# Kernel tuning notes

Hardware: AMD Instinct MI355X
Metric: run time of the kernel (lower is better)

Reference implementation:

```python
import jax, jax.numpy as jnp
import numpy as np

N = 100000   # num_nodes
E = 1250000  # num_edges
D = 64       # embedding_dim
L = 3        # num_layers


def setup_inputs() -> dict:
    key = jax.random.key(0)
    k1, k2, k3, k4 = jax.random.split(key, 4)
    edge_index = jax.random.randint(k1, (2, E), 0, N, dtype=jnp.int64)
    edge_label_index = jax.random.randint(k2, (2, E), 0, N, dtype=jnp.int64)
    # xavier_uniform init of Embedding(N, D)
    bound = float(np.sqrt(6.0 / (N + D)))
    emb_weight = jax.random.uniform(k3, (N, D), jnp.float32, -bound, bound)
    alpha = jnp.full((L + 1,), 1.0 / (L + 1), dtype=jnp.float32)
    return {"edge_index": edge_index, "edge_label_index": edge_label_index,
            "emb_weight": emb_weight, "alpha": alpha}


def reference(edge_index, edge_label_index, emb_weight, alpha):
    src, dst = edge_index[0], edge_index[1]
    n = emb_weight.shape[0]
    # gcn_norm (LGConv, no self-loops): deg over destination, sym normalization
    deg = jax.ops.segment_sum(jnp.ones(src.shape[0], emb_weight.dtype), dst, num_segments=n)
    dis = jnp.where(deg > 0, jax.lax.rsqrt(jnp.where(deg > 0, deg, 1.0)), 0.0)
    w = dis[src] * dis[dst]  # [E]

    weights = jax.nn.softmax(alpha)  # [L+1]
    x = emb_weight
    out = x * weights[0]
    for i in range(L):
        # LGConv: out[dst] += norm * x[src]
        x = jax.ops.segment_sum(w[:, None] * x[src], dst, num_segments=n)
        out = out + x * weights[i + 1]

    # predict_link_embedding: per-edge dot product
    return (out[edge_label_index[0]] * out[edge_label_index[1]]).sum(axis=-1)
```

## Files before the change

kernel.cpp:

```cpp
#include <hip/hip_runtime.h>
#include <math.h>

#define DIM 64
#define PART_T 4096
#define BK_SHIFT 9
#define BK_SPAN 512
#define BK_CAP 8192
#define BK_PAD 2048
#define BK_REG (BK_CAP + BK_PAD)

typedef _Float16 half8 __attribute__((ext_vector_type(8)));


__device__ __forceinline__ half8 shfl_xor_h8(half8 v, int mask) {
    int4 iv;
    __builtin_memcpy(&iv, &v, 16);
    iv.x = __shfl_xor(iv.x, mask, 64);
    iv.y = __shfl_xor(iv.y, mask, 64);
    iv.z = __shfl_xor(iv.z, mask, 64);
    iv.w = __shfl_xor(iv.w, mask, 64);
    half8 r;
    __builtin_memcpy(&r, &iv, 16);
    return r;
}

__device__ __forceinline__ half8 dpp_ror8_h8(half8 v) {
    int4 iv;
    __builtin_memcpy(&iv, &v, 16);
    int4 r;
    r.x = __builtin_amdgcn_update_dpp(0, iv.x, 0x128, 0xF, 0xF, true);
    r.y = __builtin_amdgcn_update_dpp(0, iv.y, 0x128, 0xF, 0xF, true);
    r.z = __builtin_amdgcn_update_dpp(0, iv.z, 0x128, 0xF, 0xF, true);
    r.w = __builtin_amdgcn_update_dpp(0, iv.w, 0x128, 0xF, 0xF, true);
    half8 out;
    __builtin_memcpy(&out, &r, 16);
    return out;
}

__device__ __forceinline__ float dpp_sum8_f32(float v) {
    int x = __float_as_int(v);
    v += __int_as_float(__builtin_amdgcn_update_dpp(0, x, 0xB1, 0xF, 0xF, true));
    x = __float_as_int(v);
    v += __int_as_float(__builtin_amdgcn_update_dpp(0, x, 0x4E, 0xF, 0xF, true));
    x = __float_as_int(v);
    v += __int_as_float(__builtin_amdgcn_update_dpp(0, x, 0x141, 0xF, 0xF, true));
    return v;
}

__device__ __forceinline__ int wave_incl_scan(int v) {
    int lane = threadIdx.x & 63;
    #pragma unroll
    for (int d = 1; d < 64; d <<= 1) {
        int n = __shfl_up(v, d, 64);
        if (lane >= d) v += n;
    }
    return v;
}

__device__ __forceinline__ int block_scan_excl(int v, int* wsum) {
    int incl = wave_incl_scan(v);
    int w = threadIdx.x >> 6;
    if ((threadIdx.x & 63) == 63) wsum[w] = incl;
    __syncthreads();
    int offset = 0;
    #pragma unroll
    for (int i = 0; i < 3; ++i) offset += (i < w) ? wsum[i] : 0;
    return offset + incl - v;
}


__global__ void init_kernel(int* __restrict__ gcursor, int K,
                            half8* __restrict__ g0, half8* __restrict__ g1,
                            half8* __restrict__ g2, int N) {
    int t = threadIdx.x;
    if (t < K) gcursor[t] = t * BK_CAP;
    if (t < 8) {
        half8 z = (half8)(_Float16)0;
        g0[(size_t)N * 8 + t] = z;
        g1[(size_t)N * 8 + t] = z;
        g2[(size_t)N * 8 + t] = z;
    }
}


__global__ void part_kernel(const int* __restrict__ src, const int* __restrict__ dst,
                            int* __restrict__ gcursor, unsigned int* __restrict__ part,
                            int E, int K) {
    __shared__ unsigned int tmp_rec[PART_T];
    __shared__ unsigned int reord[PART_T];
    __shared__ unsigned char tmp_bkt[PART_T];
    __shared__ unsigned char tmp_bkt2[PART_T];
    __shared__ int hist[256];
    __shared__ int lstart[256];
    __shared__ int cursor[256];
    __shared__ int gbase[256];
    __shared__ int wsum[4];
    int t = threadIdx.x;
    int tile = blockIdx.x * PART_T;
    int n = E - tile; if (n > PART_T) n = PART_T;

    hist[t] = 0;
    __syncthreads();

    for (int i = t; i < n; i += 256) {
        int s = src[tile + i];
        int d = dst[tile + i];
        int b = d >> BK_SHIFT;
        tmp_rec[i] = (unsigned int)s | ((unsigned int)(d & (BK_SPAN - 1)) << 17);
        tmp_bkt[i] = (unsigned char)b;
        atomicAdd(&hist[b], 1);
    }
    __syncthreads();

    int hv = hist[t];
    int excl = block_scan_excl(hv, wsum);
    lstart[t] = excl;
    cursor[t] = excl;
    if (t < K && hv > 0) gbase[t] = atomicAdd(&gcursor[t], hv);
    __syncthreads();

    for (int i = t; i < n; i += 256) {
        int b = tmp_bkt[i];
        int r = atomicAdd(&cursor[b], 1);
        reord[r] = tmp_rec[i];
        tmp_bkt2[r] = (unsigned char)b;
    }
    __syncthreads();

    for (int i = t; i < n; i += 256) {
        int b = tmp_bkt2[i];
        part[gbase[b] + (i - lstart[b])] = reord[i];
    }
}


__global__ void csr_kernel(const unsigned int* __restrict__ part, const int* __restrict__ gcursor,
                           int2* __restrict__ prange, int* __restrict__ csr_src,
                           float* __restrict__ dis,
                           const float* __restrict__ emb, half8* __restrict__ g0, int N) {
    __shared__ int h[BK_SPAN];
    __shared__ int pfx[BK_SPAN + 1];
    __shared__ float sdis[BK_SPAN];
    __shared__ int wsum[4];
    int b = blockIdx.x;
    int t = threadIdx.x;
    int pbase = b * BK_CAP;
    int cnt   = gcursor[b] - pbase;
    int qbase = b * BK_REG;
    int nodeBase = b << BK_SHIFT;

    h[t] = 0; h[t + 256] = 0;
    __syncthreads();

    for (int j = t; j < cnt; j += 256) {
        unsigned int rec = part[pbase + j];
        atomicAdd(&h[rec >> 17], 1);
    }
    __syncthreads();

    int d0 = h[2 * t], d1 = h[2 * t + 1];
    {
        float f0 = d0 > 0 ? rsqrtf((float)d0) : 0.0f;
        float f1 = d1 > 0 ? rsqrtf((float)d1) : 0.0f;
        int i0 = nodeBase + 2 * t, i1 = i0 + 1;
        if (i0 < N) dis[i0] = f0;
        if (i1 < N) dis[i1] = f1;
        sdis[2 * t] = f0;
        sdis[2 * t + 1] = f1;
    }
    int p0 = (d0 + 3) & ~3;
    int p1 = (d1 + 3) & ~3;
    int excl = block_scan_excl(p0 + p1, wsum);
    pfx[2 * t]     = excl;
    pfx[2 * t + 1] = excl + p0;
    h[2 * t]       = excl;
    h[2 * t + 1]   = excl + p0;
    if (t == 255) pfx[BK_SPAN] = excl + p0 + p1;
    __syncthreads();

    #pragma unroll
    for (int k = 0; k < 2; ++k) {
        int i = t + k * 256;
        int idx = nodeBase + i;
        if (idx < N) prange[idx] = make_int2(qbase + pfx[i], qbase + pfx[i + 1]);
    }
    __syncthreads();

    for (int j = t; j < cnt; j += 256) {
        unsigned int rec = part[pbase + j];
        int dl = (int)(rec >> 17);
        int s  = (int)(rec & 0x1FFFFu);
        int p = atomicAdd(&h[dl], 1);
        csr_src[qbase + p] = s;
    }
    __syncthreads();

    #pragma unroll
    for (int k = 0; k < 2; ++k) {
        int i = t + k * 256;
        int endp = pfx[i + 1];
        for (int p = h[i]; p < endp; ++p) csr_src[qbase + p] = N;
    }

    const float4* e4 = (const float4*)emb;
    int nloc = N - nodeBase;
    if (nloc > BK_SPAN) nloc = BK_SPAN;
    int lim = nloc * 8;
    for (int j = t; j < lim; j += 256) {
        int r = j >> 3;
        int v = nodeBase + r;
        float dv = sdis[r];
        float4 a = e4[(size_t)v * 16 + (size_t)(j & 7) * 2];
        float4 c = e4[(size_t)v * 16 + (size_t)(j & 7) * 2 + 1];
        half8 hh;
        hh[0] = (_Float16)(dv * a.x); hh[1] = (_Float16)(dv * a.y);
        hh[2] = (_Float16)(dv * a.z); hh[3] = (_Float16)(dv * a.w);
        hh[4] = (_Float16)(dv * c.x); hh[5] = (_Float16)(dv * c.y);
        hh[6] = (_Float16)(dv * c.z); hh[7] = (_Float16)(dv * c.w);
        g0[(size_t)v * 8 + (j & 7)] = hh;
    }
}


__device__ __forceinline__ void softmax4(const float* __restrict__ alpha, float* w) {
    float a0 = alpha[0], a1 = alpha[1], a2 = alpha[2], a3 = alpha[3];
    float m = fmaxf(fmaxf(a0, a1), fmaxf(a2, a3));
    float e0 = expf(a0 - m), e1 = expf(a1 - m), e2 = expf(a2 - m), e3 = expf(a3 - m);
    float s = 1.0f / (e0 + e1 + e2 + e3);
    w[0] = e0 * s; w[1] = e1 * s; w[2] = e2 * s; w[3] = e3 * s;
}

__global__ void spmm_kernel(const int2* __restrict__ prange, const int* __restrict__ csr_src,
                            const float* __restrict__ dis,
                            const half8* __restrict__ gin, half8* __restrict__ gout, int N) {
    int lane = threadIdx.x & 63;
    int wave = blockIdx.x * (blockDim.x >> 6) + (threadIdx.x >> 6);
    int v = wave * 2 + (lane >> 5);
    int slot = (lane >> 3) & 3;
    int sub  = lane & 7;
    bool valid = v < N;
    int beg = 0, end = 0;
    if (valid) { int2 pr = prange[v]; beg = pr.x; end = pr.y; }
    const int4* csr4 = (const int4*)csr_src;
    half8 acc0 = (half8)(_Float16)0;
    half8 acc1 = (half8)(_Float16)0;
    for (int j = beg + slot * 4; j < end; j += 16) {
        int4 c = csr4[j >> 2];
        acc0 = acc0 + gin[c.x * 8 + sub];
        acc1 = acc1 + gin[c.y * 8 + sub];
        acc0 = acc0 + gin[c.z * 8 + sub];
        acc1 = acc1 + gin[c.w * 8 + sub];
    }
    half8 acc = acc0 + acc1;
    acc = acc + dpp_ror8_h8(acc);
    acc = acc + shfl_xor_h8(acc, 16);
    if (valid && (lane & 31) < 8) {
        float d = dis[v];
        float d2 = d * d;
        half8 o;
        #pragma unroll
        for (int k = 0; k < 8; ++k) o[k] = (_Float16)(d2 * (float)acc[k]);
        gout[v * 8 + sub] = o;
    }
}

__global__ void spmm_final_kernel(const int2* __restrict__ prange, const int* __restrict__ csr_src,
                                  const float* __restrict__ dis,
                                  const float* __restrict__ emb, const half8* __restrict__ g1,
                                  const half8* __restrict__ g2, half8* __restrict__ out,
                                  const float* __restrict__ alpha, int N) {
    int lane = threadIdx.x & 63;
    int wave = blockIdx.x * (blockDim.x >> 6) + (threadIdx.x >> 6);
    int v = wave * 2 + (lane >> 5);
    int slot = (lane >> 3) & 3;
    int sub  = lane & 7;
    bool valid = v < N;
    int beg = 0, end = 0;
    if (valid) { int2 pr = prange[v]; beg = pr.x; end = pr.y; }
    const int4* csr4 = (const int4*)csr_src;
    half8 acc0 = (half8)(_Float16)0;
    half8 acc1 = (half8)(_Float16)0;
    for (int j = beg + slot * 4; j < end; j += 16) {
        int4 c = csr4[j >> 2];
        acc0 = acc0 + g2[c.x * 8 + sub];
        acc1 = acc1 + g2[c.y * 8 + sub];
        acc0 = acc0 + g2[c.z * 8 + sub];
        acc1 = acc1 + g2[c.w * 8 + sub];
    }
    half8 acc = acc0 + acc1;
    acc = acc + dpp_ror8_h8(acc);
    acc = acc + shfl_xor_h8(acc, 16);
    if (valid && (lane & 31) < 8) {
        float w[4];
        softmax4(alpha, w);
        float d  = dis[v];
        float iv = d > 0.0f ? 1.0f / d : 0.0f;
        const float4* e4 = (const float4*)emb;
        float4 ea = e4[v * 16 + sub * 2];
        float4 eb = e4[v * 16 + sub * 2 + 1];
        half8 h1 = g1[v * 8 + sub];
        half8 h2 = g2[v * 8 + sub];
        float ef[8] = {ea.x, ea.y, ea.z, ea.w, eb.x, eb.y, eb.z, eb.w};
        half8 o;
        #pragma unroll
        for (int k = 0; k < 8; ++k) {
            float x1 = (float)h1[k] * iv;
            float x2 = (float)h2[k] * iv;
            float x3 = d * (float)acc[k];
            float val = w[0] * ef[k] + w[1] * x1 + w[2] * x2 + w[3] * x3;
            o[k] = (_Float16)val;
        }
        out[v * 8 + sub] = o;
    }
}

__global__ void dot_kernel(const int* __restrict__ a, const int* __restrict__ b,
                           const half8* __restrict__ out, float* __restrict__ res, int E) {
    long long g = (long long)blockIdx.x * blockDim.x + threadIdx.x;
    int e   = (int)(g >> 3);
    int sub = (int)(g & 7);
    if (e >= E) return;
    int ia = a[e];
    int ib = b[e];
    half8 va = out[ia * 8 + sub];
    half8 vb = out[ib * 8 + sub];
#if __has_builtin(__builtin_amdgcn_fdot2)
    float v = 0.f;
    v = __builtin_amdgcn_fdot2(__builtin_shufflevector(va, va, 0, 1),
                               __builtin_shufflevector(vb, vb, 0, 1), v, false);
    v = __builtin_amdgcn_fdot2(__builtin_shufflevector(va, va, 2, 3),
                               __builtin_shufflevector(vb, vb, 2, 3), v, false);
    v = __builtin_amdgcn_fdot2(__builtin_shufflevector(va, va, 4, 5),
                               __builtin_shufflevector(vb, vb, 4, 5), v, false);
    v = __builtin_amdgcn_fdot2(__builtin_shufflevector(va, va, 6, 7),
                               __builtin_shufflevector(vb, vb, 6, 7), v, false);
#else
    float v = 0.f;
    #pragma unroll
    for (int k = 0; k < 8; ++k) v += (float)va[k] * (float)vb[k];
#endif
    v = dpp_sum8_f32(v);
    if (sub == 0) res[e] = v;
}


static inline size_t align256(size_t x) { return (x + 255) & ~(size_t)255; }

extern "C" void kernel_launch(void* const* d_in, const int* in_sizes, int n_in,
                              void* d_out, int out_size, void* d_ws, size_t ws_size,
                              hipStream_t stream) {
    const int* edge_index = (const int*)d_in[0];
    const int* edge_label = (const int*)d_in[1];
    const float* emb      = (const float*)d_in[2];
    const float* alpha    = (const float*)d_in[3];

    const int E = in_sizes[0] / 2;
    const int N = in_sizes[2] / DIM;
    const int K = (N + BK_SPAN - 1) >> BK_SHIFT;

    const int* src = edge_index;
    const int* dst = edge_index + E;
    const int* la  = edge_label;
    const int* lb  = edge_label + E;

    char* ws = (char*)d_ws;
    size_t off = 0;
    float* dis     = (float*)(ws + off); off = align256(off + (size_t)N * 4);
    int2*  prange  = (int2*)(ws + off);  off = align256(off + (size_t)N * 8);
    int*   gcursor = (int*)(ws + off);   off = align256(off + (size_t)256 * 4);
    unsigned int* part = (unsigned int*)(ws + off); off = align256(off + (size_t)K * BK_CAP * 4);
    int*   csr_src = (int*)(ws + off);   off = align256(off + (size_t)K * BK_REG * 4);
    half8* g0      = (half8*)(ws + off); off = align256(off + (size_t)(N + 1) * DIM * 2);
    half8* g1      = (half8*)(ws + off); off = align256(off + (size_t)(N + 1) * DIM * 2);
    half8* g2      = (half8*)(ws + off); off = align256(off + (size_t)(N + 1) * DIM * 2);
    half8* outbuf  = g0;
    (void)ws_size;

    const int B = 256;
    const int gridT = (E + PART_T - 1) / PART_T;

    init_kernel<<<1, B, 0, stream>>>(gcursor, K, g0, g1, g2, N);

    part_kernel<<<gridT, B, 0, stream>>>(src, dst, gcursor, part, E, K);

    csr_kernel<<<K, B, 0, stream>>>(part, gcursor, prange, csr_src, dis, emb, g0, N);

    const int nodesPerBlock = (B / 64) * 2;
    const int gridS = (N + nodesPerBlock - 1) / nodesPerBlock;
    spmm_kernel<<<gridS, B, 0, stream>>>(prange, csr_src, dis, g0, g1, N);
    spmm_kernel<<<gridS, B, 0, stream>>>(prange, csr_src, dis, g1, g2, N);
    spmm_final_kernel<<<gridS, B, 0, stream>>>(prange, csr_src, dis, emb, g1, g2,
                                               outbuf, alpha, N);

    const long long dthreads = (long long)E * 8;
    const int gridD = (int)((dthreads + B - 1) / B);
    dot_kernel<<<gridD, B, 0, stream>>>(la, lb, outbuf, (float*)d_out, E);
}
```

Measured before the change: 230.6 us.

## Scatter partition records directly and widen CSR build blocks to 1024 threads

```diff
diff --git a/kernel.cpp b/kernel.cpp
--- a/kernel.cpp
+++ b/kernel.cpp
@@ -2,12 +2,13 @@
 #include <math.h>
 
 #define DIM 64
-#define PART_T 4096
+#define PART_T 2048
 #define BK_SHIFT 9
 #define BK_SPAN 512
 #define BK_CAP 8192
 #define BK_PAD 2048
 #define BK_REG (BK_CAP + BK_PAD)
+#define CSR_T 1024
 
 typedef _Float16 half8 __attribute__((ext_vector_type(8)));
 
@@ -68,6 +69,18 @@
     return offset + incl - v;
 }
 
+template <int NW>
+__device__ __forceinline__ int block_scan_excl_n(int v, int* wsum) {
+    int incl = wave_incl_scan(v);
+    int w = threadIdx.x >> 6;
+    if ((threadIdx.x & 63) == 63) wsum[w] = incl;
+    __syncthreads();
+    int offset = 0;
+    #pragma unroll
+    for (int i = 0; i < NW - 1; ++i) offset += (i < w) ? wsum[i] : 0;
+    return offset + incl - v;
+}
+
 
 __global__ void init_kernel(int* __restrict__ gcursor, int K,
                             half8* __restrict__ g0, half8* __restrict__ g1,
@@ -87,9 +100,7 @@
                             int* __restrict__ gcursor, unsigned int* __restrict__ part,
                             int E, int K) {
     __shared__ unsigned int tmp_rec[PART_T];
-    __shared__ unsigned int reord[PART_T];
     __shared__ unsigned char tmp_bkt[PART_T];
-    __shared__ unsigned char tmp_bkt2[PART_T];
     __shared__ int hist[256];
     __shared__ int lstart[256];
     __shared__ int cursor[256];
@@ -122,26 +133,20 @@
     for (int i = t; i < n; i += 256) {
         int b = tmp_bkt[i];
         int r = atomicAdd(&cursor[b], 1);
-        reord[r] = tmp_rec[i];
-        tmp_bkt2[r] = (unsigned char)b;
-    }
-    __syncthreads();
-
-    for (int i = t; i < n; i += 256) {
-        int b = tmp_bkt2[i];
-        part[gbase[b] + (i - lstart[b])] = reord[i];
-    }
-}
-
-
-__global__ void csr_kernel(const unsigned int* __restrict__ part, const int* __restrict__ gcursor,
-                           int2* __restrict__ prange, int* __restrict__ csr_src,
-                           float* __restrict__ dis,
-                           const float* __restrict__ emb, half8* __restrict__ g0, int N) {
+        part[gbase[b] + (r - lstart[b])] = tmp_rec[i];
+    }
+}
+
+
+__global__ __launch_bounds__(CSR_T)
+void csr_kernel(const unsigned int* __restrict__ part, const int* __restrict__ gcursor,
+                int2* __restrict__ prange, int* __restrict__ csr_src,
+                float* __restrict__ dis,
+                const float* __restrict__ emb, half8* __restrict__ g0, int N) {
     __shared__ int h[BK_SPAN];
     __shared__ int pfx[BK_SPAN + 1];
     __shared__ float sdis[BK_SPAN];
-    __shared__ int wsum[4];
+    __shared__ int wsum[CSR_T / 64];
     int b = blockIdx.x;
     int t = threadIdx.x;
     int pbase = b * BK_CAP;
@@ -149,44 +154,38 @@
     int qbase = b * BK_REG;
     int nodeBase = b << BK_SHIFT;
 
-    h[t] = 0; h[t + 256] = 0;
-    __syncthreads();
-
-    for (int j = t; j < cnt; j += 256) {
+    if (t < BK_SPAN) h[t] = 0;
+    __syncthreads();
+
+    for (int j = t; j < cnt; j += CSR_T) {
         unsigned int rec = part[pbase + j];
         atomicAdd(&h[rec >> 17], 1);
     }
     __syncthreads();
 
-    int d0 = h[2 * t], d1 = h[2 * t + 1];
-    {
+    int d0 = (t < BK_SPAN) ? h[t] : 0;
+    if (t < BK_SPAN) {
         float f0 = d0 > 0 ? rsqrtf((float)d0) : 0.0f;
-        float f1 = d1 > 0 ? rsqrtf((float)d1) : 0.0f;
-        int i0 = nodeBase + 2 * t, i1 = i0 + 1;
+        int i0 = nodeBase + t;
         if (i0 < N) dis[i0] = f0;
-        if (i1 < N) dis[i1] = f1;
-        sdis[2 * t] = f0;
-        sdis[2 * t + 1] = f1;
+        sdis[t] = f0;
     }
     int p0 = (d0 + 3) & ~3;
-    int p1 = (d1 + 3) & ~3;
-    int excl = block_scan_excl(p0 + p1, wsum);
-    pfx[2 * t]     = excl;
-    pfx[2 * t + 1] = excl + p0;
-    h[2 * t]       = excl;
-    h[2 * t + 1]   = excl + p0;
-    if (t == 255) pfx[BK_SPAN] = excl + p0 + p1;
-    __syncthreads();
-
-    #pragma unroll
-    for (int k = 0; k < 2; ++k) {
-        int i = t + k * 256;
-        int idx = nodeBase + i;
-        if (idx < N) prange[idx] = make_int2(qbase + pfx[i], qbase + pfx[i + 1]);
-    }
-    __syncthreads();
-
-    for (int j = t; j < cnt; j += 256) {
+    int excl = block_scan_excl_n<CSR_T / 64>(p0, wsum);
+    if (t < BK_SPAN) {
+        pfx[t] = excl;
+        h[t]   = excl;
+    }
+    if (t == BK_SPAN - 1) pfx[BK_SPAN] = excl + p0;
+    __syncthreads();
+
+    if (t < BK_SPAN) {
+        int idx = nodeBase + t;
+        if (idx < N) prange[idx] = make_int2(qbase + pfx[t], qbase + pfx[t + 1]);
+    }
+    __syncthreads();
+
+    for (int j = t; j < cnt; j += CSR_T) {
         unsigned int rec = part[pbase + j];
         int dl = (int)(rec >> 17);
         int s  = (int)(rec & 0x1FFFFu);
@@ -195,18 +194,16 @@
     }
     __syncthreads();
 
-    #pragma unroll
-    for (int k = 0; k < 2; ++k) {
-        int i = t + k * 256;
-        int endp = pfx[i + 1];
-        for (int p = h[i]; p < endp; ++p) csr_src[qbase + p] = N;
+    if (t < BK_SPAN) {
+        int endp = pfx[t + 1];
+        for (int p = h[t]; p < endp; ++p) csr_src[qbase + p] = N;
     }
 
     const float4* e4 = (const float4*)emb;
     int nloc = N - nodeBase;
     if (nloc > BK_SPAN) nloc = BK_SPAN;
     int lim = nloc * 8;
-    for (int j = t; j < lim; j += 256) {
+    for (int j = t; j < lim; j += CSR_T) {
         int r = j >> 3;
         int v = nodeBase + r;
         float dv = sdis[r];
@@ -383,7 +380,7 @@
 
     part_kernel<<<gridT, B, 0, stream>>>(src, dst, gcursor, part, E, K);
 
-    csr_kernel<<<K, B, 0, stream>>>(part, gcursor, prange, csr_src, dis, emb, g0, N);
+    csr_kernel<<<K, CSR_T, 0, stream>>>(part, gcursor, prange, csr_src, dis, emb, g0, N);
 
     const int nodesPerBlock = (B / 64) * 2;
     const int gridS = (N + nodesPerBlock - 1) / nodesPerBlock;
```

Measured after the change: 230.4 us. No clear change (-0.1%).
